# Kernel tuning notes

Measured on AMD Instinct MI355X. Metric: run time of the kernel, lower is better.

Reference implementation:

```python
import jax, jax.numpy as jnp
import numpy as np

HEADS = 4
DIM_HEAD = 128


def setup_inputs() -> dict:
    key = jax.random.key(0)
    k1, k2, k3, k4, k5 = jax.random.split(key, 5)
    dim = 256
    f, h, w = 8, 14, 14
    inner = HEADS * DIM_HEAD
    scale = DIM_HEAD ** -0.5
    fmap = jax.random.normal(k1, (8, dim, f, h, w), dtype=jnp.float32)
    # Conv3d 1x1x1, no bias -> plain channel matmul weight [3*inner, dim]
    W_qkv = jax.random.normal(k2, (3 * inner, dim), dtype=jnp.float32) * (dim ** -0.5)
    pos_f = jax.random.normal(k3, (f, DIM_HEAD), dtype=jnp.float32) * scale
    pos_h = jax.random.normal(k4, (h, DIM_HEAD), dtype=jnp.float32) * scale
    pos_w = jax.random.normal(k5, (w, DIM_HEAD), dtype=jnp.float32) * scale
    return {"fmap": fmap, "W_qkv": W_qkv, "pos_f": pos_f, "pos_h": pos_h, "pos_w": pos_w}


def reference(fmap, W_qkv, pos_f, pos_h, pos_w):
    b, c, f, h, w = fmap.shape
    n = f * h * w
    scale = DIM_HEAD ** -0.5
    # 1x1x1 Conv3d == channel matmul
    qkv = jnp.einsum('bcfhw,oc->bofhw', fmap, W_qkv)  # [b, 3*inner, f, h, w]
    q, k, v = jnp.split(qkv, 3, axis=1)
    # 'b (h d) x y z -> b h (x y z) d'
    def to_heads(t):
        return t.reshape(b, HEADS, DIM_HEAD, n).transpose(0, 1, 3, 2)
    q, k, v = to_heads(q), to_heads(k), to_heads(v)
    q = q * scale
    # additive absolute positional embedding [n, d]
    emb = (pos_f[:, None, None, :] + pos_h[None, :, None, :] + pos_w[None, None, :, :]).reshape(n, DIM_HEAD)
    sim = jnp.einsum('bhid,bhjd->bhij', q, k) + jnp.einsum('bhid,jd->bhij', q, emb)
    attn = jax.nn.softmax(sim, axis=-1)
    out = jnp.einsum('bhij,bhjd->bhid', attn, v)  # [b, heads, n, d]
    # 'b h (x y z) d -> b (h d) x y z'
    out = out.transpose(0, 1, 3, 2).reshape(b, HEADS * DIM_HEAD, f, h, w)
    return out
```

## Files before the change

### kernel.cpp

```cpp
#include <hip/hip_runtime.h>
#include <hip/hip_bf16.h>
#include <cstdint>

#define NPOS 1568
#define NQPAD 1664
#define NKVT 25
#define DHEAD 128
#define DIM 256
#define SCALE_Q (0.08838834764831845f * 1.4426950408889634f)

typedef __bf16 bf16x8 __attribute__((ext_vector_type(8)));
typedef float f32x4 __attribute__((ext_vector_type(4)));
typedef float f32x16 __attribute__((ext_vector_type(16)));
typedef unsigned short u16;
typedef u16 u16x8 __attribute__((ext_vector_type(8)));

__device__ __forceinline__ unsigned cvtpk(float a, float b) {
  unsigned r;
  asm("v_cvt_pk_bf16_f32 %0, %1, %2" : "=v"(r) : "v"(a), "v"(b));
  return r;
}

__device__ __forceinline__ f32x16 zero16() {
  f32x16 v;
#pragma unroll
  for (int i = 0; i < 16; ++i) v[i] = 0.f;
  return v;
}

__global__ __launch_bounds__(256) void emb_kernel(
    const float* __restrict__ pf, const float* __restrict__ ph,
    const float* __restrict__ pw, float* __restrict__ emb) {
  int idx = blockIdx.x * 256 + threadIdx.x;
  int pos = idx >> 7, d = idx & 127;
  int jf = pos / 196; int r = pos - jf * 196; int jh = r / 14; int jw = r - jh * 14;
  emb[idx] = pf[jf * 128 + d] + ph[jh * 128 + d] + pw[jw * 128 + d];
}

__global__ __launch_bounds__(256) void wconv_kernel(
    const float* __restrict__ W, u16* __restrict__ Wbf) {
  int i8 = (blockIdx.x * 256 + threadIdx.x) * 8;
  float4 f0 = *(const float4*)(W + i8);
  float4 f1 = *(const float4*)(W + i8 + 4);
  union { unsigned u[4]; u16x8 v; } o;
  o.u[0] = cvtpk(f0.x, f0.y); o.u[1] = cvtpk(f0.z, f0.w);
  o.u[2] = cvtpk(f1.x, f1.y); o.u[3] = cvtpk(f1.z, f1.w);
  *(u16x8*)(Wbf + i8) = o.v;
}

__global__ __launch_bounds__(256) void ftrans_kernel(
    const float* __restrict__ fmap, u16* __restrict__ fmapT) {
  __shared__ float t[64][68];
  const int tid = threadIdx.x;
  const int pos0 = blockIdx.x * 64, c0 = blockIdx.y * 64, b = blockIdx.z;
  const int cl = tid >> 3, p8 = (tid & 7) * 8;
  const bool pv = (pos0 + p8) < NPOS;
#pragma unroll
  for (int half = 0; half < 2; ++half) {
    int c = cl + half * 32;
    float4 f0 = {0.f, 0.f, 0.f, 0.f}, f1 = {0.f, 0.f, 0.f, 0.f};
    if (pv) {
      const float* src = fmap + ((size_t)(b * DIM + c0 + c)) * NPOS + pos0 + p8;
      f0 = *(const float4*)src;
      f1 = *(const float4*)(src + 4);
    }
    *(float4*)&t[c][p8] = f0;
    *(float4*)&t[c][p8 + 4] = f1;
  }
  __syncthreads();
  const int pl = tid >> 2, c16 = (tid & 3) * 16;
  const int gpos = pos0 + pl;
  union { unsigned u[8]; } o;
  if (gpos < NPOS) {
#pragma unroll
    for (int i = 0; i < 8; ++i) o.u[i] = cvtpk(t[c16 + 2 * i][pl], t[c16 + 2 * i + 1][pl]);
  } else {
#pragma unroll
    for (int i = 0; i < 8; ++i) o.u[i] = 0;
  }
  u16* dst = fmapT + ((size_t)b * NQPAD + gpos) * DIM + c0 + c16;
  *(uint4*)(dst) = *(uint4*)&o.u[0];
  *(uint4*)(dst + 8) = *(uint4*)&o.u[4];
}

__global__ __launch_bounds__(256, 4) void proj_kernel(
    const u16* __restrict__ Wbf, const u16* __restrict__ fmapT,
    const float* __restrict__ emb, u16* __restrict__ qws, char* __restrict__ tiles) {
  __shared__ float ot[64][132];
  const int tid = threadIdx.x;
  const int lane = tid & 63, w = tid >> 6;
  const int l15 = lane & 15, g = lane >> 4;
  const int wid = blockIdx.x;
  const int b = wid & 7;
  const int gq = wid >> 3;
  const int o0 = (gq / 13) * 128;
  const int pos0 = (gq % 13) * 128;
  const int wo = (w & 1) * 64, wp = (w >> 1) * 64;

  f32x4 acc[4][4];
#pragma unroll
  for (int i = 0; i < 4; ++i)
#pragma unroll
    for (int j = 0; j < 4; ++j) acc[i][j] = (f32x4){0.f, 0.f, 0.f, 0.f};

  const u16* Ab = Wbf + (size_t)(o0 + wo + l15) * DIM + g * 8;
  const u16* Bb = fmapT + ((size_t)b * NQPAD + pos0 + wp + l15) * DIM + g * 8;
#pragma unroll 2
  for (int c0 = 0; c0 < DIM; c0 += 32) {
    bf16x8 a[4], bb[4];
#pragma unroll
    for (int t = 0; t < 4; ++t) a[t] = *(const bf16x8*)(Ab + (size_t)t * 16 * DIM + c0);
#pragma unroll
    for (int t = 0; t < 4; ++t) bb[t] = *(const bf16x8*)(Bb + (size_t)t * 16 * DIM + c0);
#pragma unroll
    for (int i = 0; i < 4; ++i)
#pragma unroll
      for (int j = 0; j < 4; ++j)
        acc[i][j] = __builtin_amdgcn_mfma_f32_16x16x32_bf16(a[i], bb[j], acc[i][j], 0, 0, 0);
  }

  const int sec = o0 >> 9, head = (o0 >> 7) & 3, bh = b * 4 + head;

  if (sec < 2) {
#pragma unroll
    for (int ph = 0; ph < 2; ++ph) {
      __syncthreads();
      if (wp == ph * 64) {
#pragma unroll
        for (int i = 0; i < 4; ++i)
#pragma unroll
          for (int j = 0; j < 4; ++j)
#pragma unroll
            for (int r = 0; r < 4; ++r)
              ot[j * 16 + l15][wo + i * 16 + 4 * g + r] = acc[i][j][r];
      }
      __syncthreads();
      const int pl = tid >> 2, c32 = (tid & 3) * 32;
      const int gpos = pos0 + ph * 64 + pl;
      float v[32];
#pragma unroll
      for (int i = 0; i < 32; ++i) v[i] = ot[pl][c32 + i];
      if (sec == 0) {
#pragma unroll
        for (int q = 0; q < 4; ++q) {
          union { unsigned u[4]; u16x8 h; } o8;
#pragma unroll
          for (int i = 0; i < 4; ++i)
            o8.u[i] = cvtpk(v[q * 8 + 2 * i] * SCALE_Q, v[q * 8 + 2 * i + 1] * SCALE_Q);
          *(u16x8*)(qws + ((size_t)bh * NQPAD + gpos) * DHEAD + c32 + q * 8) = o8.h;
        }
      } else {
        if (gpos < NKVT * 64) {
          if (gpos < NPOS) {
            const float* eb = emb + (size_t)gpos * DHEAD + c32;
#pragma unroll
            for (int i = 0; i < 8; ++i) {
              float4 e = *(const float4*)(eb + i * 4);
              v[i * 4 + 0] += e.x; v[i * 4 + 1] += e.y;
              v[i * 4 + 2] += e.z; v[i * 4 + 3] += e.w;
            }
          }
          const int jt = gpos >> 6, jl = gpos & 63;
          const int grp = jl >> 5, jl31 = jl & 31;
          const int l31s = (jl31 & 0x13) | ((jl31 & 4) << 1) | ((jl31 & 8) >> 1);
          char* tb = tiles + ((size_t)(bh * NKVT + jt)) * 32768 + grp * 8192;
#pragma unroll
          for (int q = 0; q < 4; ++q) {
            union { unsigned u[4]; u16x8 h; } o8;
#pragma unroll
            for (int i = 0; i < 4; ++i)
              o8.u[i] = cvtpk(v[q * 8 + 2 * i], v[q * 8 + 2 * i + 1]);
            const int c = c32 + q * 8;
            const int kk = c >> 4, hi = (c >> 3) & 1;
            *(u16x8*)(tb + kk * 1024 + (hi * 32 + l31s) * 16) = o8.h;
          }
        }
      }
    }
  } else {
#pragma unroll
    for (int ch = 0; ch < 2; ++ch) {
      __syncthreads();
      if (wo == ch * 64) {
#pragma unroll
        for (int i = 0; i < 4; ++i)
#pragma unroll
          for (int j = 0; j < 4; ++j)
#pragma unroll
            for (int r = 0; r < 4; ++r)
              ot[i * 16 + 4 * g + r][wp + j * 16 + l15] = acc[i][j][r];
      }
      __syncthreads();
      const int dl = tid >> 2, p32 = (tid & 3) * 32;
      const int d = ch * 64 + dl;
      const int gp = pos0 + p32;
      float v[32];
#pragma unroll
      for (int i = 0; i < 32; ++i) v[i] = ot[dl][p32 + i];
      if (gp < NKVT * 64) {
        const int jt = gp >> 6, jl0 = gp & 63;
        const int dt = d >> 5, dl31 = d & 31;
        char* tb = tiles + ((size_t)(bh * NKVT + jt)) * 32768 + 16384;
#pragma unroll
        for (int q = 0; q < 4; ++q) {
          union { unsigned u[4]; u16x8 h; } o8;
#pragma unroll
          for (int i = 0; i < 4; ++i)
            o8.u[i] = cvtpk(v[q * 8 + 2 * i], v[q * 8 + 2 * i + 1]);
          const int jl = jl0 + q * 8;
          const int grp = jl >> 5, kj = (jl >> 4) & 1, hi2 = (jl >> 3) & 1;
          *(u16x8*)(tb + grp * 8192 + dt * 2048 + kj * 1024 + (hi2 * 32 + dl31) * 16) = o8.h;
        }
      }
    }
  }
}

__global__ __launch_bounds__(256, 2) void attn_kernel(
    const u16* __restrict__ qws, const char* __restrict__ tiles,
    float* __restrict__ out) {
  __shared__ float ml[2 * 64 * 2];
  __shared__ float cx[32 * 128];
  const int tid = threadIdx.x;
  const int lane = tid & 63, w = tid >> 6;
  const int qw = w & 1, grp = w >> 1;
  const int l31 = lane & 31, hi = lane >> 5;
  const int wid = blockIdx.x;
  const int bh = (wid & 7) * 4 + (wid >> 3) / 26;
  const int qt = (wid >> 3) % 26;
  const int b = bh >> 2, h = bh & 3;
  const int q0 = qt * 64;

  bf16x8 qf[8];
  {
    const u16* qp = qws + ((size_t)bh * NQPAD + q0 + qw * 32 + l31) * DHEAD + 8 * hi;
#pragma unroll
    for (int kk = 0; kk < 8; ++kk) qf[kk] = *(const bf16x8*)(qp + kk * 16);
  }

  f32x16 oacc[4];
#pragma unroll
  for (int dt = 0; dt < 4; ++dt) oacc[dt] = zero16();
  float m = -1e30f, l = 0.f;

  const char* kb = tiles + (size_t)bh * NKVT * 32768 + grp * 8192 + lane * 16;
  const char* vb = kb + 16384;

  for (int jt = 0; jt < NKVT; ++jt) {
    if (grp == 0 || jt < NKVT - 1) {
      bf16x8 ka[8];
#pragma unroll
      for (int kk = 0; kk < 8; ++kk) ka[kk] = *(const bf16x8*)(kb + kk * 1024);
      bf16x8 va[4][2];
#pragma unroll
      for (int dt = 0; dt < 4; ++dt)
#pragma unroll
        for (int kj = 0; kj < 2; ++kj)
          va[dt][kj] = *(const bf16x8*)(vb + dt * 2048 + kj * 1024);

      f32x16 sc = zero16();
#pragma unroll
      for (int kk = 0; kk < 8; ++kk)
        sc = __builtin_amdgcn_mfma_f32_32x32x16_bf16(ka[kk], qf[kk], sc, 0, 0, 0);

      float pm = -1e30f;
#pragma unroll
      for (int i = 0; i < 16; ++i) pm = fmaxf(pm, sc[i]);
      pm = fmaxf(pm, __shfl_xor(pm, 32));
      if (!__all(pm <= m + 8.f)) {
        float mn = fmaxf(m, pm);
        float al = exp2f(m - mn);
        m = mn;
        l *= al;
#pragma unroll
        for (int dt = 0; dt < 4; ++dt)
#pragma unroll
          for (int i = 0; i < 16; ++i) oacc[dt][i] *= al;
      }
      float lac = 0.f;
#pragma unroll
      for (int i = 0; i < 16; ++i) { sc[i] = exp2f(sc[i] - m); lac += sc[i]; }
      l += lac;

      union { unsigned u[4]; bf16x8 v; } pb0, pb1;
      pb0.u[0] = cvtpk(sc[0], sc[1]);   pb0.u[1] = cvtpk(sc[2], sc[3]);
      pb0.u[2] = cvtpk(sc[4], sc[5]);   pb0.u[3] = cvtpk(sc[6], sc[7]);
      pb1.u[0] = cvtpk(sc[8], sc[9]);   pb1.u[1] = cvtpk(sc[10], sc[11]);
      pb1.u[2] = cvtpk(sc[12], sc[13]); pb1.u[3] = cvtpk(sc[14], sc[15]);
#pragma unroll
      for (int dt = 0; dt < 4; ++dt) {
        oacc[dt] = __builtin_amdgcn_mfma_f32_32x32x16_bf16(va[dt][0], pb0.v, oacc[dt], 0, 0, 0);
        oacc[dt] = __builtin_amdgcn_mfma_f32_32x32x16_bf16(va[dt][1], pb1.v, oacc[dt], 0, 0, 0);
      }
    }
    kb += 32768; vb += 32768;
  }

  float lt = l + __shfl_xor(l, 32);
  if (grp == 1) {
    ml[(qw * 64 + lane) * 2 + 0] = m;
    ml[(qw * 64 + lane) * 2 + 1] = lt;
  }
  __syncthreads();
  float fA = 0.f, fB = 0.f;
  if (grp == 0) {
    float mB = ml[(qw * 64 + lane) * 2 + 0];
    float lB = ml[(qw * 64 + lane) * 2 + 1];
    float ms = fmaxf(m, mB);
    float aA = exp2f(m - ms), aB = exp2f(mB - ms);
    float inv = 1.f / (lt * aA + lB * aB);
    fA = aA * inv; fB = aB * inv;
  }
  const int q = q0 + qw * 32 + l31;
  float* ob = out + (size_t)(b * 512 + h * 128) * NPOS + q;
#pragma unroll
  for (int ch = 0; ch < 2; ++ch) {
    __syncthreads();
    if (grp == 1) {
#pragma unroll
      for (int k = 0; k < 2; ++k)
#pragma unroll
        for (int i = 0; i < 16; ++i)
          cx[(k * 16 + i) * 128 + qw * 64 + lane] = oacc[ch * 2 + k][i];
    }
    __syncthreads();
    if (grp == 0 && q < NPOS) {
#pragma unroll
      for (int k = 0; k < 2; ++k) {
        const int dt = ch * 2 + k;
#pragma unroll
        for (int r = 0; r < 16; ++r) {
          float vB = cx[(k * 16 + r) * 128 + qw * 64 + lane];
          float vo = oacc[dt][r] * fA + vB * fB;
          int d = dt * 32 + (r & 3) + 8 * (r >> 2) + 4 * hi;
          ob[(size_t)d * NPOS] = vo;
        }
      }
    }
  }
}

extern "C" void kernel_launch(void* const* d_in, const int* in_sizes, int n_in,
                              void* d_out, int out_size, void* d_ws, size_t ws_size,
                              hipStream_t stream) {
  const float* fmap = (const float*)d_in[0];
  const float* W    = (const float*)d_in[1];
  const float* pf   = (const float*)d_in[2];
  const float* ph   = (const float*)d_in[3];
  const float* pw   = (const float*)d_in[4];
  float* out = (float*)d_out;

  char* ws = (char*)d_ws;
  const size_t QSZ = (size_t)32 * NQPAD * DHEAD * 2;
  u16* qws    = (u16*)ws;
  char* tiles = ws + QSZ;

  char* oscr = (char*)d_out;
  const size_t FSZ = (size_t)8 * NQPAD * DIM * 2;
  const size_t WSZ = (size_t)1536 * DIM * 2;
  u16* fmapT = (u16*)oscr;
  u16* Wbf   = (u16*)(oscr + FSZ);
  float* emb = (float*)(oscr + FSZ + WSZ);

  emb_kernel<<<dim3(784), dim3(256), 0, stream>>>(pf, ph, pw, emb);
  wconv_kernel<<<dim3(192), dim3(256), 0, stream>>>(W, Wbf);
  ftrans_kernel<<<dim3(26, 4, 8), dim3(256), 0, stream>>>(fmap, fmapT);
  proj_kernel<<<dim3(1248), dim3(256), 0, stream>>>(Wbf, fmapT, emb, qws, tiles);
  attn_kernel<<<dim3(832), dim3(256), 0, stream>>>(qws, tiles, out);
}
```

Measured before the change: 145.4 us.

## Double-buffer projection GEMM loads and coalesce tile epilogue stores

```diff
diff --git a/kernel.cpp b/kernel.cpp
--- a/kernel.cpp
+++ b/kernel.cpp
@@ -83,7 +83,7 @@
   *(uint4*)(dst + 8) = *(uint4*)&o.u[4];
 }
 
-__global__ __launch_bounds__(256, 4) void proj_kernel(
+__global__ __launch_bounds__(256, 3) void proj_kernel(
     const u16* __restrict__ Wbf, const u16* __restrict__ fmapT,
     const float* __restrict__ emb, u16* __restrict__ qws, char* __restrict__ tiles) {
   __shared__ float ot[64][132];
@@ -105,18 +105,28 @@
 
   const u16* Ab = Wbf + (size_t)(o0 + wo + l15) * DIM + g * 8;
   const u16* Bb = fmapT + ((size_t)b * NQPAD + pos0 + wp + l15) * DIM + g * 8;
-#pragma unroll 2
-  for (int c0 = 0; c0 < DIM; c0 += 32) {
-    bf16x8 a[4], bb[4];
-#pragma unroll
-    for (int t = 0; t < 4; ++t) a[t] = *(const bf16x8*)(Ab + (size_t)t * 16 * DIM + c0);
-#pragma unroll
-    for (int t = 0; t < 4; ++t) bb[t] = *(const bf16x8*)(Bb + (size_t)t * 16 * DIM + c0);
+
+  bf16x8 a[2][4], bb[2][4];
+#pragma unroll
+  for (int t = 0; t < 4; ++t) {
+    a[0][t]  = *(const bf16x8*)(Ab + (size_t)t * 16 * DIM);
+    bb[0][t] = *(const bf16x8*)(Bb + (size_t)t * 16 * DIM);
+  }
+#pragma unroll
+  for (int st = 0; st < 8; ++st) {
+    const int cur = st & 1, nxt = cur ^ 1;
+    if (st < 7) {
+#pragma unroll
+      for (int t = 0; t < 4; ++t) {
+        a[nxt][t]  = *(const bf16x8*)(Ab + (size_t)t * 16 * DIM + (st + 1) * 32);
+        bb[nxt][t] = *(const bf16x8*)(Bb + (size_t)t * 16 * DIM + (st + 1) * 32);
+      }
+    }
 #pragma unroll
     for (int i = 0; i < 4; ++i)
 #pragma unroll
       for (int j = 0; j < 4; ++j)
-        acc[i][j] = __builtin_amdgcn_mfma_f32_16x16x32_bf16(a[i], bb[j], acc[i][j], 0, 0, 0);
+        acc[i][j] = __builtin_amdgcn_mfma_f32_16x16x32_bf16(a[cur][i], bb[cur][j], acc[i][j], 0, 0, 0);
   }
 
   const int sec = o0 >> 9, head = (o0 >> 7) & 3, bh = b * 4 + head;
@@ -135,44 +145,43 @@
               ot[j * 16 + l15][wo + i * 16 + 4 * g + r] = acc[i][j][r];
       }
       __syncthreads();
-      const int pl = tid >> 2, c32 = (tid & 3) * 32;
-      const int gpos = pos0 + ph * 64 + pl;
-      float v[32];
-#pragma unroll
-      for (int i = 0; i < 32; ++i) v[i] = ot[pl][c32 + i];
       if (sec == 0) {
 #pragma unroll
-        for (int q = 0; q < 4; ++q) {
+        for (int it = 0; it < 4; ++it) {
+          const int p = it * 16 + (tid >> 4), d0 = (tid & 15) * 8;
+          const int gpos = pos0 + ph * 64 + p;
+          const float* r = &ot[p][d0];
           union { unsigned u[4]; u16x8 h; } o8;
 #pragma unroll
           for (int i = 0; i < 4; ++i)
-            o8.u[i] = cvtpk(v[q * 8 + 2 * i] * SCALE_Q, v[q * 8 + 2 * i + 1] * SCALE_Q);
-          *(u16x8*)(qws + ((size_t)bh * NQPAD + gpos) * DHEAD + c32 + q * 8) = o8.h;
+            o8.u[i] = cvtpk(r[2 * i] * SCALE_Q, r[2 * i + 1] * SCALE_Q);
+          *(u16x8*)(qws + ((size_t)bh * NQPAD + gpos) * DHEAD + d0) = o8.h;
         }
       } else {
-        if (gpos < NKVT * 64) {
-          if (gpos < NPOS) {
-            const float* eb = emb + (size_t)gpos * DHEAD + c32;
-#pragma unroll
-            for (int i = 0; i < 8; ++i) {
-              float4 e = *(const float4*)(eb + i * 4);
-              v[i * 4 + 0] += e.x; v[i * 4 + 1] += e.y;
-              v[i * 4 + 2] += e.z; v[i * 4 + 3] += e.w;
+        const int jt = (pos0 >> 6) + ph;
+        if (jt < NKVT) {
+          char* tb = tiles + ((size_t)(bh * NKVT + jt)) * 32768;
+#pragma unroll
+          for (int u = 0; u < 4; ++u) {
+            const int L = u * 256 + tid;
+            const int grp = L >> 9, kk = (L >> 6) & 7, s = L & 63;
+            const int sl = s & 31, hi2 = s >> 5;
+            const int rr = (sl & 0x13) | ((sl & 4) << 1) | ((sl & 8) >> 1);
+            const int row = grp * 32 + rr;
+            const int d0 = kk * 16 + hi2 * 8;
+            const int gpos = pos0 + ph * 64 + row;
+            float vv[8];
+#pragma unroll
+            for (int i = 0; i < 8; ++i) vv[i] = ot[row][d0 + i];
+            if (gpos < NPOS) {
+              const float* eb = emb + (size_t)gpos * DHEAD + d0;
+#pragma unroll
+              for (int i = 0; i < 8; ++i) vv[i] += eb[i];
             }
-          }
-          const int jt = gpos >> 6, jl = gpos & 63;
-          const int grp = jl >> 5, jl31 = jl & 31;
-          const int l31s = (jl31 & 0x13) | ((jl31 & 4) << 1) | ((jl31 & 8) >> 1);
-          char* tb = tiles + ((size_t)(bh * NKVT + jt)) * 32768 + grp * 8192;
-#pragma unroll
-          for (int q = 0; q < 4; ++q) {
-            union { unsigned u[4]; u16x8 h; } o8;
-#pragma unroll
-            for (int i = 0; i < 4; ++i)
-              o8.u[i] = cvtpk(v[q * 8 + 2 * i], v[q * 8 + 2 * i + 1]);
-            const int c = c32 + q * 8;
-            const int kk = c >> 4, hi = (c >> 3) & 1;
-            *(u16x8*)(tb + kk * 1024 + (hi * 32 + l31s) * 16) = o8.h;
+            union { unsigned u4[4]; u16x8 h; } o8;
+#pragma unroll
+            for (int i = 0; i < 4; ++i) o8.u4[i] = cvtpk(vv[2 * i], vv[2 * i + 1]);
+            *(u16x8*)(tb + grp * 8192 + kk * 1024 + s * 16) = o8.h;
           }
         }
       }
@@ -191,25 +200,24 @@
               ot[i * 16 + 4 * g + r][wp + j * 16 + l15] = acc[i][j][r];
       }
       __syncthreads();
-      const int dl = tid >> 2, p32 = (tid & 3) * 32;
-      const int d = ch * 64 + dl;
-      const int gp = pos0 + p32;
-      float v[32];
-#pragma unroll
-      for (int i = 0; i < 32; ++i) v[i] = ot[dl][p32 + i];
-      if (gp < NKVT * 64) {
-        const int jt = gp >> 6, jl0 = gp & 63;
-        const int dt = d >> 5, dl31 = d & 31;
-        char* tb = tiles + ((size_t)(bh * NKVT + jt)) * 32768 + 16384;
-#pragma unroll
-        for (int q = 0; q < 4; ++q) {
-          union { unsigned u[4]; u16x8 h; } o8;
-#pragma unroll
-          for (int i = 0; i < 4; ++i)
-            o8.u[i] = cvtpk(v[q * 8 + 2 * i], v[q * 8 + 2 * i + 1]);
-          const int jl = jl0 + q * 8;
-          const int grp = jl >> 5, kj = (jl >> 4) & 1, hi2 = (jl >> 3) & 1;
-          *(u16x8*)(tb + grp * 8192 + dt * 2048 + kj * 1024 + (hi2 * 32 + dl31) * 16) = o8.h;
+      const int jt0 = pos0 >> 6;
+#pragma unroll
+      for (int u = 0; u < 4; ++u) {
+        const int L = u * 256 + tid;
+        const int jtl = L >> 9, grp = (L >> 8) & 1, dtl = (L >> 7) & 1;
+        const int kj = (L >> 6) & 1, s = L & 63;
+        const int jt = jt0 + jtl;
+        if (jt < NKVT) {
+          const int drow = dtl * 32 + (s & 31);
+          const int pcol = jtl * 64 + grp * 32 + kj * 16 + (s >> 5) * 8;
+          float vv[8];
+#pragma unroll
+          for (int i = 0; i < 8; ++i) vv[i] = ot[drow][pcol + i];
+          union { unsigned u4[4]; u16x8 h; } o8;
+#pragma unroll
+          for (int i = 0; i < 4; ++i) o8.u4[i] = cvtpk(vv[2 * i], vv[2 * i + 1]);
+          *(u16x8*)(tiles + ((size_t)(bh * NKVT + jt)) * 32768 + 16384 +
+                    grp * 8192 + (2 * ch + dtl) * 2048 + kj * 1024 + s * 16) = o8.h;
         }
       }
     }
```

Measured after the change: 144.1 us. No clear change (-0.9%).
